# Performance work log

Hardware: AMD Instinct MI355X
Metric: run time of the kernel (lower is better)

Reference implementation:

```python
import jax, jax.numpy as jnp
import numpy as np

N_NODES = 100000


def setup_inputs() -> dict:
    key = jax.random.key(0)
    k1, k2, k3 = jax.random.split(key, 3)
    embedding = jax.random.normal(k1, (N_NODES, 128), dtype=jnp.float32)
    # xavier-ish scale for 128-dim fan-in
    weights = jax.random.normal(k2, (2, 4, 128, 128), dtype=jnp.float32) * 0.088
    biases = jnp.zeros((2, 4, 128), dtype=jnp.float32)
    edges = jax.random.randint(k3, (4, 2, 150000), 0, N_NODES, dtype=jnp.int32)
    return {"embedding": embedding, "weights": weights, "biases": biases, "edges": edges}


def _hetero_conv(h, W, b, edges, n_nodes):
    """HeteroGraphConv(mean) over R relations; each GraphConv uses norm='both'.
    h: [N, d_in], W: [R, d_in, d_h], b: [R, d_h], edges: [R, 2, E]."""

    def per_rel(e, Wr, br):
        src, dst = e[0], e[1]
        ones = jnp.ones(src.shape, dtype=h.dtype)
        deg_out = jnp.maximum(jax.ops.segment_sum(ones, src, num_segments=n_nodes), 1.0)
        deg_in = jnp.maximum(jax.ops.segment_sum(ones, dst, num_segments=n_nodes), 1.0)
        # D_src^{-1/2} X W
        x = h * jax.lax.rsqrt(deg_out)[:, None]
        m = x @ Wr  # [N, d_h]
        # gather along edges, scatter-add to dst (A @ m)
        agg = jax.ops.segment_sum(m[src], dst, num_segments=n_nodes)
        return agg * jax.lax.rsqrt(deg_in)[:, None] + br

    outs = jax.vmap(per_rel)(edges, W, b)  # [R, N, d_h]
    return outs.mean(axis=0)


def reference(embedding, weights, biases, edges):
    n_nodes = embedding.shape[0]
    num_layers = weights.shape[0]
    h = embedding
    for i in range(num_layers):
        out = _hetero_conv(h, weights[i], biases[i], edges, n_nodes)
        out = jax.nn.leaky_relu(out, negative_slope=0.2)
        if i > 0:
            out = out + h  # residual (hidden == in, slice [:, :hidden] is identity)
        h = out
    return h
```

## Files before the change

kernel.cpp:

```cpp
#include <hip/hip_runtime.h>
#include <cstdint>
#include <cstddef>

#define N_NODES 100000
#define D 128
#define R 4
#define NE 150000
#define LAYERS 2
#define NROWS (R * N_NODES)
#define CAP 16
#define TILES (N_NODES / 16)
#define GRID 256
#define TPB 512

typedef __attribute__((ext_vector_type(8))) short bf16x8;
typedef __attribute__((ext_vector_type(4))) float f32x4;
typedef __attribute__((ext_vector_type(4))) int i32x4;
typedef __attribute__((ext_vector_type(4))) unsigned short u16x4;

__device__ __forceinline__ unsigned short f2bf(float x) {
  union { float f; unsigned int u; } v; v.f = x;
  unsigned int u = v.u;
  return (unsigned short)((u + 0x7fffu + ((u >> 16) & 1u)) >> 16);
}
__device__ __forceinline__ float bf2f(unsigned short u) {
  union { unsigned int i; float f; } v; v.i = ((unsigned int)u) << 16;
  return v.f;
}

__global__ void count_kernel(const int* __restrict__ edges, int* __restrict__ deg_i) {
  int e = blockIdx.x * blockDim.x + threadIdx.x;
  int r = blockIdx.y;
  if (e >= NE) return;
  int src = edges[(size_t)(r * 2) * NE + e];
  atomicAdd(&deg_i[r * N_NODES + src], 1);
}

__global__ void fill_kernel(const int* __restrict__ edges, const int* __restrict__ deg_i,
                            int* __restrict__ cursor, int2* __restrict__ rec) {
  int e = blockIdx.x * blockDim.x + threadIdx.x;
  int r = blockIdx.y;
  if (e >= NE) return;
  int src = edges[(size_t)(r * 2) * NE + e];
  int dst = edges[(size_t)(r * 2 + 1) * NE + e];
  float sc = rsqrtf(fmaxf((float)deg_i[r * N_NODES + src], 1.0f));
  int rowg = r * N_NODES + dst;
  int slot = atomicAdd(&cursor[rowg], 1);
  if (slot < CAP) rec[(size_t)rowg * CAP + slot] = make_int2(src, __float_as_int(sc));
}

__global__ void prep_kernel(const float* __restrict__ emb, const float* __restrict__ W,
                            const float* __restrict__ biases, const int* __restrict__ cursor,
                            unsigned short* __restrict__ hb, unsigned short* __restrict__ Wt,
                            float* __restrict__ bmean, float* __restrict__ s_in) {
  int t = blockIdx.x * blockDim.x + threadIdx.x;
  if (t < N_NODES * D / 4) {
    f32x4 v = *(const f32x4*)(emb + (size_t)t * 4);
    u16x4 o;
#pragma unroll
    for (int j = 0; j < 4; ++j) o[j] = f2bf(v[j]);
    *(u16x4*)(hb + (size_t)t * 4) = o;
  }
  if (t < LAYERS * R * D * D) {
    int k = t & 127;
    int c = (t >> 7) & 127;
    int lr = t >> 14;
    Wt[((size_t)lr << 14) | (c << 7) | k] = f2bf(W[((size_t)lr << 14) | (k << 7) | c]);
  }
  if (t < NROWS) s_in[t] = rsqrtf(fmaxf((float)cursor[t], 1.0f));
  if (t < LAYERS * D) {
    int l = t >> 7, cc = t & 127;
    float s = 0.f;
    for (int r = 0; r < R; ++r) s += biases[((size_t)l * R + r) * D + cc];
    bmean[t] = s * 0.25f;
  }
}

__global__ __launch_bounds__(TPB, 2) void fused_kernel(
    const unsigned short* __restrict__ hb,
    const int2* __restrict__ rec,
    const int* __restrict__ cnt,
    const float* __restrict__ s_in,
    const unsigned short* __restrict__ Wt,
    const float* __restrict__ bmean,
    const unsigned short* __restrict__ resid_bf,
    float* __restrict__ out_f,
    unsigned short* __restrict__ out_bf) {
  __shared__ unsigned short t_lds[2][R * 4 * 64 * 8];
  const int w = threadIdx.x >> 6;
  const int lane = threadIdx.x & 63;
  const int m = lane & 15;
  const int q = lane >> 4;
  const int bid = blockIdx.x;
  const int nt = (TILES - bid + GRID - 1) / GRID;

  if (w < 4) {
    const int r = w;
    for (int it = 0; it < nt + 1; ++it) {
      if (it < nt) {
        const int tile = bid + it * GRID;
        const int rowg = r * N_NODES + tile * 16 + m;
        const int2* rp = rec + (size_t)rowg * CAP;
        int n = cnt[rowg];
        n = (n > CAP) ? CAP : n;
        i32x4 r01 = *(const i32x4*)(rp);
        i32x4 r23 = *(const i32x4*)(rp + 2);
        int   srcs[4] = { r01.x, r01.z, r23.x, r23.z };
        float scs[4]  = { __int_as_float(r01.y), __int_as_float(r01.w),
                          __int_as_float(r23.y), __int_as_float(r23.w) };
        float accf[4][8];
#pragma unroll
        for (int ks = 0; ks < 4; ++ks)
#pragma unroll
          for (int j = 0; j < 8; ++j) accf[ks][j] = 0.f;
#pragma unroll
        for (int e = 0; e < 4; ++e) {
          const unsigned short* hp = hb + (size_t)srcs[e] * D + q * 8;
#pragma unroll
          for (int ks = 0; ks < 4; ++ks) {
            bf16x8 a = *(const bf16x8*)(hp + ks * 32);
#pragma unroll
            for (int j = 0; j < 8; ++j)
              accf[ks][j] += scs[e] * bf2f((unsigned short)a[j]);
          }
        }
        for (int i = 4; i < n; i += 2) {
          i32x4 rr = *(const i32x4*)(rp + i);
          float c0 = __int_as_float(rr.y), c1 = __int_as_float(rr.w);
          const unsigned short* h0 = hb + (size_t)rr.x * D + q * 8;
          const unsigned short* h1 = hb + (size_t)rr.z * D + q * 8;
#pragma unroll
          for (int ks = 0; ks < 4; ++ks) {
            bf16x8 a0 = *(const bf16x8*)(h0 + ks * 32);
            bf16x8 a1 = *(const bf16x8*)(h1 + ks * 32);
#pragma unroll
            for (int j = 0; j < 8; ++j)
              accf[ks][j] += c0 * bf2f((unsigned short)a0[j]) + c1 * bf2f((unsigned short)a1[j]);
          }
        }
        unsigned short* dstp = &t_lds[it & 1][(((r * 4) << 6) + lane) * 8];
#pragma unroll
        for (int ks = 0; ks < 4; ++ks) {
          union { bf16x8 v; unsigned short s[8]; } u;
#pragma unroll
          for (int j = 0; j < 8; ++j) u.s[j] = f2bf(accf[ks][j]);
          *(bf16x8*)(dstp + (ks << 6) * 8) = u.v;
        }
      }
      __syncthreads();
    }
  } else {
    const int cw = w - 4;
    bf16x8 breg[R][4][2];
#pragma unroll
    for (int r = 0; r < R; ++r) {
      const unsigned short* wr = Wt + ((size_t)r << 14);
#pragma unroll
      for (int ks = 0; ks < 4; ++ks)
#pragma unroll
        for (int c = 0; c < 2; ++c) {
          int ct = cw * 2 + c;
          breg[r][ks][c] = *(const bf16x8*)(wr + ((ct * 16 + m) << 7) + ks * 32 + q * 8);
        }
    }
    for (int it = 0; it < nt + 1; ++it) {
      if (it > 0) {
        const int tile = bid + (it - 1) * GRID;
        const int pb = (it - 1) & 1;
        float oacc[2][4];
#pragma unroll
        for (int c = 0; c < 2; ++c)
#pragma unroll
          for (int i = 0; i < 4; ++i) oacc[c][i] = 0.f;
#pragma unroll
        for (int r = 0; r < R; ++r) {
          f32x4 acc2[2];
#pragma unroll
          for (int c = 0; c < 2; ++c) acc2[c] = (f32x4){0.f, 0.f, 0.f, 0.f};
#pragma unroll
          for (int ks = 0; ks < 4; ++ks) {
            bf16x8 a = *(const bf16x8*)&t_lds[pb][(((r * 4 + ks) << 6) + lane) * 8];
#pragma unroll
            for (int c = 0; c < 2; ++c)
              acc2[c] = __builtin_amdgcn_mfma_f32_16x16x32_bf16(a, breg[r][ks][c], acc2[c], 0, 0, 0);
          }
          f32x4 s = *(const f32x4*)(s_in + (size_t)r * N_NODES + tile * 16 + q * 4);
#pragma unroll
          for (int c = 0; c < 2; ++c)
#pragma unroll
            for (int i = 0; i < 4; ++i) oacc[c][i] += s[i] * acc2[c][i];
        }
#pragma unroll
        for (int c = 0; c < 2; ++c) {
          int colx = (cw * 2 + c) * 16 + m;
          float bm = bmean[colx];
#pragma unroll
          for (int i = 0; i < 4; ++i) {
            int row = tile * 16 + q * 4 + i;
            float v = oacc[c][i] * 0.25f + bm;
            v = (v >= 0.f) ? v : 0.2f * v;
            if (resid_bf) v += bf2f(resid_bf[(size_t)row * D + colx]);
            if (out_f) out_f[(size_t)row * D + colx] = v;
            else       out_bf[(size_t)row * D + colx] = f2bf(v);
          }
        }
      }
      __syncthreads();
    }
  }
}

extern "C" void kernel_launch(void* const* d_in, const int* in_sizes, int n_in,
                              void* d_out, int out_size, void* d_ws, size_t ws_size,
                              hipStream_t stream) {
  const float* emb    = (const float*)d_in[0];
  const float* W      = (const float*)d_in[1];
  const float* biases = (const float*)d_in[2];
  const int*   edges  = (const int*)d_in[3];
  float* out = (float*)d_out;
  char* ws = (char*)d_ws;

  size_t off = 0;
  auto alloc = [&](size_t bytes) { size_t o = off; off += (bytes + 255) & ~255ull; return o; };
  int* ints      = (int*)(ws + alloc((size_t)2 * NROWS * 4));
  int* deg_i     = ints;
  int* cursor    = ints + NROWS;
  int2* rec      = (int2*)(ws + alloc((size_t)NROWS * CAP * 8));
  size_t zero_bytes = off;
  float* s_in    = (float*)(ws + alloc((size_t)NROWS * 4));
  unsigned short* hb  = (unsigned short*)(ws + alloc((size_t)N_NODES * D * 2));
  unsigned short* hb2 = (unsigned short*)(ws + alloc((size_t)N_NODES * D * 2));
  unsigned short* Wt  = (unsigned short*)(ws + alloc((size_t)LAYERS * R * D * D * 2));
  float* bmean   = (float*)(ws + alloc((size_t)LAYERS * D * 4));
  (void)ws_size;

  hipMemsetAsync(ws, 0, zero_bytes, stream);
  count_kernel<<<dim3((NE + 255) / 256, R), 256, 0, stream>>>(edges, deg_i);
  fill_kernel<<<dim3((NE + 255) / 256, R), 256, 0, stream>>>(edges, deg_i, cursor, rec);
  prep_kernel<<<(N_NODES * D / 4 + 255) / 256, 256, 0, stream>>>(
      emb, W, biases, cursor, hb, Wt, bmean, s_in);

  fused_kernel<<<GRID, TPB, 0, stream>>>(
      hb, rec, cursor, s_in, Wt, bmean, nullptr, nullptr, hb2);
  fused_kernel<<<GRID, TPB, 0, stream>>>(
      hb2, rec, cursor, s_in, Wt + (size_t)R * D * D, bmean + D, hb2, out, nullptr);
}
```

Before: 338.0 us.

## Software-pipeline edge gathers, split CSR into compact head and overflow, merge prep kernels

The gather warps now issue the next tile's neighbour-row loads into registers (double-buffered A/B state) before accumulating the current tile, which hides gather latency. Edge records are split into a compact tile-major 4-slot head array plus an overflow array, so the zeroed workspace is smaller and the common-case record reads are contiguous. Degree counting is folded into the embedding/weight prep kernel, and the s_in precompute is replaced by computing rsqrt from counts inline, which removes a kernel launch and a pass. Barriers become raw s_barrier with explicit lgkmcnt waits. The cost is much higher register pressure in the gather warps.

```diff
diff --git a/kernel.cpp b/kernel.cpp
--- a/kernel.cpp
+++ b/kernel.cpp
@@ -9,6 +9,7 @@
 #define LAYERS 2
 #define NROWS (R * N_NODES)
 #define CAP 16
+#define OVFS 12
 #define TILES (N_NODES / 16)
 #define GRID 256
 #define TPB 512
@@ -28,16 +29,41 @@
   return v.f;
 }
 
-__global__ void count_kernel(const int* __restrict__ edges, int* __restrict__ deg_i) {
-  int e = blockIdx.x * blockDim.x + threadIdx.x;
-  int r = blockIdx.y;
-  if (e >= NE) return;
-  int src = edges[(size_t)(r * 2) * NE + e];
-  atomicAdd(&deg_i[r * N_NODES + src], 1);
+__global__ void prep1_kernel(const float* __restrict__ emb, const float* __restrict__ W,
+                             const float* __restrict__ biases, const int* __restrict__ edges,
+                             int* __restrict__ deg_i, unsigned short* __restrict__ hb,
+                             unsigned short* __restrict__ Wt, float* __restrict__ bmean) {
+  int t = blockIdx.x * blockDim.x + threadIdx.x;
+  if (t < N_NODES * D / 4) {
+    f32x4 v = *(const f32x4*)(emb + (size_t)t * 4);
+    u16x4 o;
+#pragma unroll
+    for (int j = 0; j < 4; ++j) o[j] = f2bf(v[j]);
+    *(u16x4*)(hb + (size_t)t * 4) = o;
+  }
+  if (t < NE * R) {
+    int r = t / NE;
+    int e = t - r * NE;
+    int src = edges[(size_t)(r * 2) * NE + e];
+    atomicAdd(&deg_i[r * N_NODES + src], 1);
+  }
+  if (t < LAYERS * R * D * D) {
+    int k = t & 127;
+    int c = (t >> 7) & 127;
+    int lr = t >> 14;
+    Wt[((size_t)lr << 14) | (c << 7) | k] = f2bf(W[((size_t)lr << 14) | (k << 7) | c]);
+  }
+  if (t < LAYERS * D) {
+    int l = t >> 7, cc = t & 127;
+    float s = 0.f;
+    for (int r = 0; r < R; ++r) s += biases[((size_t)l * R + r) * D + cc];
+    bmean[t] = s * 0.25f;
+  }
 }
 
 __global__ void fill_kernel(const int* __restrict__ edges, const int* __restrict__ deg_i,
-                            int* __restrict__ cursor, int2* __restrict__ rec) {
+                            int* __restrict__ cursor, int2* __restrict__ rec2,
+                            int2* __restrict__ ovf) {
   int e = blockIdx.x * blockDim.x + threadIdx.x;
   int r = blockIdx.y;
   if (e >= NE) return;
@@ -46,41 +72,114 @@
   float sc = rsqrtf(fmaxf((float)deg_i[r * N_NODES + src], 1.0f));
   int rowg = r * N_NODES + dst;
   int slot = atomicAdd(&cursor[rowg], 1);
-  if (slot < CAP) rec[(size_t)rowg * CAP + slot] = make_int2(src, __float_as_int(sc));
-}
-
-__global__ void prep_kernel(const float* __restrict__ emb, const float* __restrict__ W,
-                            const float* __restrict__ biases, const int* __restrict__ cursor,
-                            unsigned short* __restrict__ hb, unsigned short* __restrict__ Wt,
-                            float* __restrict__ bmean, float* __restrict__ s_in) {
-  int t = blockIdx.x * blockDim.x + threadIdx.x;
-  if (t < N_NODES * D / 4) {
-    f32x4 v = *(const f32x4*)(emb + (size_t)t * 4);
-    u16x4 o;
-#pragma unroll
-    for (int j = 0; j < 4; ++j) o[j] = f2bf(v[j]);
-    *(u16x4*)(hb + (size_t)t * 4) = o;
-  }
-  if (t < LAYERS * R * D * D) {
-    int k = t & 127;
-    int c = (t >> 7) & 127;
-    int lr = t >> 14;
-    Wt[((size_t)lr << 14) | (c << 7) | k] = f2bf(W[((size_t)lr << 14) | (k << 7) | c]);
-  }
-  if (t < NROWS) s_in[t] = rsqrtf(fmaxf((float)cursor[t], 1.0f));
-  if (t < LAYERS * D) {
-    int l = t >> 7, cc = t & 127;
-    float s = 0.f;
-    for (int r = 0; r < R; ++r) s += biases[((size_t)l * R + r) * D + cc];
-    bmean[t] = s * 0.25f;
-  }
-}
+  if (slot < 4) {
+    int tile = dst >> 4, mm = dst & 15;
+    rec2[(((size_t)(r * TILES + tile) * 16 + mm) << 2) + slot] = make_int2(src, __float_as_int(sc));
+  } else if (slot < CAP) {
+    ovf[(size_t)rowg * OVFS + (slot - 4)] = make_int2(src, __float_as_int(sc));
+  }
+}
+
+#define DECL_ST(P) \
+  bf16x8 P##g0, P##g1, P##g2, P##g3, P##g4, P##g5, P##g6, P##g7, \
+         P##g8, P##g9, P##g10, P##g11, P##g12, P##g13, P##g14, P##g15; \
+  float P##c0 = 0.f, P##c1 = 0.f, P##c2 = 0.f, P##c3 = 0.f; \
+  i32x4 P##tr = (i32x4){0, 0, 0, 0}; \
+  int P##n = 0
+
+#define P_LOADREC(CN, R0V, R1V, TT) do { \
+  const int2* rp_ = rec2 + (((size_t)(r * TILES + (TT)) * 16 + m) << 2); \
+  CN = cnt[r * N_NODES + (TT) * 16 + m]; \
+  R0V = *(const i32x4*)(rp_); \
+  R1V = *(const i32x4*)(rp_ + 2); \
+} while (0)
+
+#define P_ISSUE(P, CN, R0V, R1V, TT) do { \
+  int n_ = (CN) > CAP ? CAP : (CN); \
+  int a0_ = (R0V).x, a1_ = (R0V).z, a2_ = (R1V).x, a3_ = (R1V).z; \
+  float b0_ = __int_as_float((R0V).y), b1_ = __int_as_float((R0V).w); \
+  float b2_ = __int_as_float((R1V).y), b3_ = __int_as_float((R1V).w); \
+  if (n_ < 1) { a0_ = 0; b0_ = 0.f; } \
+  if (n_ < 2) { a1_ = 0; b1_ = 0.f; } \
+  if (n_ < 3) { a2_ = 0; b2_ = 0.f; } \
+  if (n_ < 4) { a3_ = 0; b3_ = 0.f; } \
+  const unsigned short* h0_ = hb + (size_t)a0_ * D + q * 8; \
+  const unsigned short* h1_ = hb + (size_t)a1_ * D + q * 8; \
+  const unsigned short* h2_ = hb + (size_t)a2_ * D + q * 8; \
+  const unsigned short* h3_ = hb + (size_t)a3_ * D + q * 8; \
+  P##g0  = *(const bf16x8*)(h0_);      P##g1  = *(const bf16x8*)(h0_ + 32); \
+  P##g2  = *(const bf16x8*)(h0_ + 64); P##g3  = *(const bf16x8*)(h0_ + 96); \
+  P##g4  = *(const bf16x8*)(h1_);      P##g5  = *(const bf16x8*)(h1_ + 32); \
+  P##g6  = *(const bf16x8*)(h1_ + 64); P##g7  = *(const bf16x8*)(h1_ + 96); \
+  P##g8  = *(const bf16x8*)(h2_);      P##g9  = *(const bf16x8*)(h2_ + 32); \
+  P##g10 = *(const bf16x8*)(h2_ + 64); P##g11 = *(const bf16x8*)(h2_ + 96); \
+  P##g12 = *(const bf16x8*)(h3_);      P##g13 = *(const bf16x8*)(h3_ + 32); \
+  P##g14 = *(const bf16x8*)(h3_ + 64); P##g15 = *(const bf16x8*)(h3_ + 96); \
+  P##c0 = b0_; P##c1 = b1_; P##c2 = b2_; P##c3 = b3_; P##n = n_; \
+  if (__builtin_expect(n_ > 4, 0)) \
+    P##tr = *(const i32x4*)(ovf + (size_t)(r * N_NODES + (TT) * 16 + m) * OVFS); \
+} while (0)
+
+#define P_ACCUM(P, TT, DSTP) do { \
+  float accf[4][8]; \
+  _Pragma("unroll") for (int k_ = 0; k_ < 4; ++k_) \
+    _Pragma("unroll") for (int j_ = 0; j_ < 8; ++j_) accf[k_][j_] = 0.f; \
+  if (__builtin_expect(P##n > 4, 0)) { \
+    bool ok_ = P##n > 5; \
+    int sA_ = P##tr.x, sB_ = ok_ ? P##tr.z : 0; \
+    float cA_ = __int_as_float(P##tr.y), cB_ = ok_ ? __int_as_float(P##tr.w) : 0.f; \
+    const unsigned short* hA_ = hb + (size_t)sA_ * D + q * 8; \
+    const unsigned short* hB_ = hb + (size_t)sB_ * D + q * 8; \
+    _Pragma("unroll") for (int k_ = 0; k_ < 4; ++k_) { \
+      bf16x8 x0_ = *(const bf16x8*)(hA_ + k_ * 32); \
+      bf16x8 x1_ = *(const bf16x8*)(hB_ + k_ * 32); \
+      _Pragma("unroll") for (int j_ = 0; j_ < 8; ++j_) \
+        accf[k_][j_] += cA_ * bf2f((unsigned short)x0_[j_]) + cB_ * bf2f((unsigned short)x1_[j_]); \
+    } \
+    const int2* op_ = ovf + (size_t)(r * N_NODES + (TT) * 16 + m) * OVFS; \
+    for (int i_ = 6; i_ < P##n; i_ += 2) { \
+      i32x4 rr_ = *(const i32x4*)(op_ + (i_ - 4)); \
+      bool o2_ = (i_ + 1) < P##n; \
+      int s0_ = rr_.x, s1_ = o2_ ? rr_.z : 0; \
+      float d0_ = __int_as_float(rr_.y), d1_ = o2_ ? __int_as_float(rr_.w) : 0.f; \
+      const unsigned short* y0_ = hb + (size_t)s0_ * D + q * 8; \
+      const unsigned short* y1_ = hb + (size_t)s1_ * D + q * 8; \
+      _Pragma("unroll") for (int k_ = 0; k_ < 4; ++k_) { \
+        bf16x8 x0_ = *(const bf16x8*)(y0_ + k_ * 32); \
+        bf16x8 x1_ = *(const bf16x8*)(y1_ + k_ * 32); \
+        _Pragma("unroll") for (int j_ = 0; j_ < 8; ++j_) \
+          accf[k_][j_] += d0_ * bf2f((unsigned short)x0_[j_]) + d1_ * bf2f((unsigned short)x1_[j_]); \
+      } \
+    } \
+  } \
+  _Pragma("unroll") for (int j_ = 0; j_ < 8; ++j_) { \
+    accf[0][j_] += P##c0 * bf2f((unsigned short)P##g0[j_])  + P##c1 * bf2f((unsigned short)P##g4[j_]) \
+                 + P##c2 * bf2f((unsigned short)P##g8[j_])  + P##c3 * bf2f((unsigned short)P##g12[j_]); \
+    accf[1][j_] += P##c0 * bf2f((unsigned short)P##g1[j_])  + P##c1 * bf2f((unsigned short)P##g5[j_]) \
+                 + P##c2 * bf2f((unsigned short)P##g9[j_])  + P##c3 * bf2f((unsigned short)P##g13[j_]); \
+    accf[2][j_] += P##c0 * bf2f((unsigned short)P##g2[j_])  + P##c1 * bf2f((unsigned short)P##g6[j_]) \
+                 + P##c2 * bf2f((unsigned short)P##g10[j_]) + P##c3 * bf2f((unsigned short)P##g14[j_]); \
+    accf[3][j_] += P##c0 * bf2f((unsigned short)P##g3[j_])  + P##c1 * bf2f((unsigned short)P##g7[j_]) \
+                 + P##c2 * bf2f((unsigned short)P##g11[j_]) + P##c3 * bf2f((unsigned short)P##g15[j_]); \
+  } \
+  _Pragma("unroll") for (int k_ = 0; k_ < 4; ++k_) { \
+    union { bf16x8 v; unsigned short s[8]; } u_; \
+    _Pragma("unroll") for (int j_ = 0; j_ < 8; ++j_) u_.s[j_] = f2bf(accf[k_][j_]); \
+    *(bf16x8*)((DSTP) + (k_ << 6) * 8) = u_.v; \
+  } \
+} while (0)
+
+#define P_BARRIER() do { \
+  asm volatile("s_waitcnt lgkmcnt(0)"); \
+  __builtin_amdgcn_sched_barrier(0); \
+  __builtin_amdgcn_s_barrier(); \
+} while (0)
 
 __global__ __launch_bounds__(TPB, 2) void fused_kernel(
     const unsigned short* __restrict__ hb,
-    const int2* __restrict__ rec,
+    const int2* __restrict__ rec2,
+    const int2* __restrict__ ovf,
     const int* __restrict__ cnt,
-    const float* __restrict__ s_in,
     const unsigned short* __restrict__ Wt,
     const float* __restrict__ bmean,
     const unsigned short* __restrict__ resid_bf,
@@ -96,59 +195,42 @@
 
   if (w < 4) {
     const int r = w;
-    for (int it = 0; it < nt + 1; ++it) {
-      if (it < nt) {
-        const int tile = bid + it * GRID;
-        const int rowg = r * N_NODES + tile * 16 + m;
-        const int2* rp = rec + (size_t)rowg * CAP;
-        int n = cnt[rowg];
-        n = (n > CAP) ? CAP : n;
-        i32x4 r01 = *(const i32x4*)(rp);
-        i32x4 r23 = *(const i32x4*)(rp + 2);
-        int   srcs[4] = { r01.x, r01.z, r23.x, r23.z };
-        float scs[4]  = { __int_as_float(r01.y), __int_as_float(r01.w),
-                          __int_as_float(r23.y), __int_as_float(r23.w) };
-        float accf[4][8];
-#pragma unroll
-        for (int ks = 0; ks < 4; ++ks)
-#pragma unroll
-          for (int j = 0; j < 8; ++j) accf[ks][j] = 0.f;
-#pragma unroll
-        for (int e = 0; e < 4; ++e) {
-          const unsigned short* hp = hb + (size_t)srcs[e] * D + q * 8;
-#pragma unroll
-          for (int ks = 0; ks < 4; ++ks) {
-            bf16x8 a = *(const bf16x8*)(hp + ks * 32);
-#pragma unroll
-            for (int j = 0; j < 8; ++j)
-              accf[ks][j] += scs[e] * bf2f((unsigned short)a[j]);
-          }
-        }
-        for (int i = 4; i < n; i += 2) {
-          i32x4 rr = *(const i32x4*)(rp + i);
-          float c0 = __int_as_float(rr.y), c1 = __int_as_float(rr.w);
-          const unsigned short* h0 = hb + (size_t)rr.x * D + q * 8;
-          const unsigned short* h1 = hb + (size_t)rr.z * D + q * 8;
-#pragma unroll
-          for (int ks = 0; ks < 4; ++ks) {
-            bf16x8 a0 = *(const bf16x8*)(h0 + ks * 32);
-            bf16x8 a1 = *(const bf16x8*)(h1 + ks * 32);
-#pragma unroll
-            for (int j = 0; j < 8; ++j)
-              accf[ks][j] += c0 * bf2f((unsigned short)a0[j]) + c1 * bf2f((unsigned short)a1[j]);
-          }
+    DECL_ST(A);
+    DECL_ST(B);
+    int cnA = 0, cnB = 0;
+    i32x4 ra0, ra1, rb0, rb1;
+
+    P_LOADREC(cnA, ra0, ra1, bid);
+    P_ISSUE(A, cnA, ra0, ra1, bid);
+    if (nt > 1) P_LOADREC(cnB, rb0, rb1, bid + GRID);
+
+    int it = 0;
+    for (;;) {
+      {
+        const int tcur = bid + it * GRID;
+        if (it + 1 < nt) {
+          P_ISSUE(B, cnB, rb0, rb1, tcur + GRID);
+          if (it + 2 < nt) P_LOADREC(cnA, ra0, ra1, tcur + 2 * GRID);
         }
         unsigned short* dstp = &t_lds[it & 1][(((r * 4) << 6) + lane) * 8];
-#pragma unroll
-        for (int ks = 0; ks < 4; ++ks) {
-          union { bf16x8 v; unsigned short s[8]; } u;
-#pragma unroll
-          for (int j = 0; j < 8; ++j) u.s[j] = f2bf(accf[ks][j]);
-          *(bf16x8*)(dstp + (ks << 6) * 8) = u.v;
-        }
+        P_ACCUM(A, tcur, dstp);
+        P_BARRIER();
+        if (++it >= nt) break;
       }
-      __syncthreads();
+      {
+        const int tcur = bid + it * GRID;
+        if (it + 1 < nt) {
+          P_ISSUE(A, cnA, ra0, ra1, tcur + GRID);
+          if (it + 2 < nt) P_LOADREC(cnB, rb0, rb1, tcur + 2 * GRID);
+        }
+        unsigned short* dstp = &t_lds[it & 1][(((r * 4) << 6) + lane) * 8];
+        P_ACCUM(B, tcur, dstp);
+        P_BARRIER();
+        if (++it >= nt) break;
+      }
     }
+    asm volatile("s_waitcnt lgkmcnt(0)");
+    __builtin_amdgcn_s_barrier();
   } else {
     const int cw = w - 4;
     bf16x8 breg[R][4][2];
@@ -184,11 +266,12 @@
             for (int c = 0; c < 2; ++c)
               acc2[c] = __builtin_amdgcn_mfma_f32_16x16x32_bf16(a, breg[r][ks][c], acc2[c], 0, 0, 0);
           }
-          f32x4 s = *(const f32x4*)(s_in + (size_t)r * N_NODES + tile * 16 + q * 4);
+          i32x4 ci = *(const i32x4*)(cnt + (size_t)r * N_NODES + tile * 16 + q * 4);
 #pragma unroll
           for (int c = 0; c < 2; ++c)
 #pragma unroll
-            for (int i = 0; i < 4; ++i) oacc[c][i] += s[i] * acc2[c][i];
+            for (int i = 0; i < 4; ++i)
+              oacc[c][i] += rsqrtf(fmaxf((float)ci[i], 1.0f)) * acc2[c][i];
         }
 #pragma unroll
         for (int c = 0; c < 2; ++c) {
@@ -205,7 +288,8 @@
           }
         }
       }
-      __syncthreads();
+      asm volatile("s_waitcnt lgkmcnt(0)");
+      __builtin_amdgcn_s_barrier();
     }
   }
 }
@@ -225,9 +309,9 @@
   int* ints      = (int*)(ws + alloc((size_t)2 * NROWS * 4));
   int* deg_i     = ints;
   int* cursor    = ints + NROWS;
-  int2* rec      = (int2*)(ws + alloc((size_t)NROWS * CAP * 8));
   size_t zero_bytes = off;
-  float* s_in    = (float*)(ws + alloc((size_t)NROWS * 4));
+  int2* rec2     = (int2*)(ws + alloc((size_t)R * TILES * 16 * 4 * 8));
+  int2* ovf      = (int2*)(ws + alloc((size_t)NROWS * OVFS * 8));
   unsigned short* hb  = (unsigned short*)(ws + alloc((size_t)N_NODES * D * 2));
   unsigned short* hb2 = (unsigned short*)(ws + alloc((size_t)N_NODES * D * 2));
   unsigned short* Wt  = (unsigned short*)(ws + alloc((size_t)LAYERS * R * D * D * 2));
@@ -235,13 +319,12 @@
   (void)ws_size;
 
   hipMemsetAsync(ws, 0, zero_bytes, stream);
-  count_kernel<<<dim3((NE + 255) / 256, R), 256, 0, stream>>>(edges, deg_i);
-  fill_kernel<<<dim3((NE + 255) / 256, R), 256, 0, stream>>>(edges, deg_i, cursor, rec);
-  prep_kernel<<<(N_NODES * D / 4 + 255) / 256, 256, 0, stream>>>(
-      emb, W, biases, cursor, hb, Wt, bmean, s_in);
+  prep1_kernel<<<(N_NODES * D / 4 + 255) / 256, 256, 0, stream>>>(
+      emb, W, biases, edges, deg_i, hb, Wt, bmean);
+  fill_kernel<<<dim3((NE + 255) / 256, R), 256, 0, stream>>>(edges, deg_i, cursor, rec2, ovf);
 
   fused_kernel<<<GRID, TPB, 0, stream>>>(
-      hb, rec, cursor, s_in, Wt, bmean, nullptr, nullptr, hb2);
+      hb, rec2, ovf, cursor, Wt, bmean, nullptr, nullptr, hb2);
   fused_kernel<<<GRID, TPB, 0, stream>>>(
-      hb2, rec, cursor, s_in, Wt + (size_t)R * D * D, bmean + D, hb2, out, nullptr);
-}
+      hb2, rec2, ovf, cursor, Wt + (size_t)R * D * D, bmean + D, hb2, out, nullptr);
+}
```

After: 363.8 us. +7.6%, slower.

## Merge all stages into one cooperative kernel with grid syncs and compact edge records

Applied to the files above, without the earlier changes.

Replaces the memset, count, fill, prep and two layer kernels with a single cooperative mega-kernel that uses grid-wide syncs between phases. Edge records are split into a compact 4-slot per-row array plus an overflow buffer, which removes the 16-slot padded reads. The first four gathers are issued up front with masking to improve memory-level parallelism. The in-degree normalisation is computed on the fly from counts instead of a precomputed array. In exchange, the setup phases now run on only 256 blocks, and each grid sync adds a cost.

```diff
diff --git a/kernel.cpp b/kernel.cpp
--- a/kernel.cpp
+++ b/kernel.cpp
@@ -1,6 +1,9 @@
 #include <hip/hip_runtime.h>
+#include <hip/hip_cooperative_groups.h>
 #include <cstdint>
 #include <cstddef>
+
+namespace cg = cooperative_groups;
 
 #define N_NODES 100000
 #define D 128
@@ -9,9 +12,11 @@
 #define LAYERS 2
 #define NROWS (R * N_NODES)
 #define CAP 16
+#define OVFS 12
 #define TILES (N_NODES / 16)
 #define GRID 256
 #define TPB 512
+#define NTH (GRID * TPB)
 
 typedef __attribute__((ext_vector_type(8))) short bf16x8;
 typedef __attribute__((ext_vector_type(4))) float f32x4;
@@ -28,64 +33,64 @@
   return v.f;
 }
 
-__global__ void count_kernel(const int* __restrict__ edges, int* __restrict__ deg_i) {
-  int e = blockIdx.x * blockDim.x + threadIdx.x;
-  int r = blockIdx.y;
-  if (e >= NE) return;
-  int src = edges[(size_t)(r * 2) * NE + e];
-  atomicAdd(&deg_i[r * N_NODES + src], 1);
-}
-
-__global__ void fill_kernel(const int* __restrict__ edges, const int* __restrict__ deg_i,
-                            int* __restrict__ cursor, int2* __restrict__ rec) {
-  int e = blockIdx.x * blockDim.x + threadIdx.x;
-  int r = blockIdx.y;
-  if (e >= NE) return;
-  int src = edges[(size_t)(r * 2) * NE + e];
-  int dst = edges[(size_t)(r * 2 + 1) * NE + e];
-  float sc = rsqrtf(fmaxf((float)deg_i[r * N_NODES + src], 1.0f));
-  int rowg = r * N_NODES + dst;
-  int slot = atomicAdd(&cursor[rowg], 1);
-  if (slot < CAP) rec[(size_t)rowg * CAP + slot] = make_int2(src, __float_as_int(sc));
-}
-
-__global__ void prep_kernel(const float* __restrict__ emb, const float* __restrict__ W,
-                            const float* __restrict__ biases, const int* __restrict__ cursor,
-                            unsigned short* __restrict__ hb, unsigned short* __restrict__ Wt,
-                            float* __restrict__ bmean, float* __restrict__ s_in) {
-  int t = blockIdx.x * blockDim.x + threadIdx.x;
-  if (t < N_NODES * D / 4) {
-    f32x4 v = *(const f32x4*)(emb + (size_t)t * 4);
+__global__ __launch_bounds__(TPB, 2) void mega_kernel(
+    const float* __restrict__ emb, const float* __restrict__ W,
+    const float* __restrict__ biases, const int* __restrict__ edges,
+    int* __restrict__ ints,
+    int2* __restrict__ rec2,
+    int2* __restrict__ ovf,
+    unsigned short* __restrict__ hb,
+    unsigned short* __restrict__ hb2,
+    unsigned short* __restrict__ Wt,
+    float* __restrict__ bmean,
+    float* __restrict__ out) {
+  cg::grid_group grid = cg::this_grid();
+  int* deg_i = ints;
+  int* cursor = ints + NROWS;
+  const int tid = blockIdx.x * TPB + threadIdx.x;
+
+  for (int i = tid; i < 2 * NROWS; i += NTH) ints[i] = 0;
+  grid.sync();
+
+  for (int i = tid; i < NE * R; i += NTH) {
+    int r = i / NE, e = i - r * NE;
+    atomicAdd(&deg_i[r * N_NODES + edges[(size_t)(r * 2) * NE + e]], 1);
+  }
+  for (int i = tid; i < N_NODES * D / 4; i += NTH) {
+    f32x4 v = *(const f32x4*)(emb + (size_t)i * 4);
     u16x4 o;
 #pragma unroll
     for (int j = 0; j < 4; ++j) o[j] = f2bf(v[j]);
-    *(u16x4*)(hb + (size_t)t * 4) = o;
-  }
-  if (t < LAYERS * R * D * D) {
-    int k = t & 127;
-    int c = (t >> 7) & 127;
-    int lr = t >> 14;
+    *(u16x4*)(hb + (size_t)i * 4) = o;
+  }
+  for (int i = tid; i < LAYERS * R * D * D; i += NTH) {
+    int k = i & 127, c = (i >> 7) & 127, lr = i >> 14;
     Wt[((size_t)lr << 14) | (c << 7) | k] = f2bf(W[((size_t)lr << 14) | (k << 7) | c]);
   }
-  if (t < NROWS) s_in[t] = rsqrtf(fmaxf((float)cursor[t], 1.0f));
-  if (t < LAYERS * D) {
-    int l = t >> 7, cc = t & 127;
+  if (tid < LAYERS * D) {
+    int l = tid >> 7, cc = tid & 127;
     float s = 0.f;
     for (int r = 0; r < R; ++r) s += biases[((size_t)l * R + r) * D + cc];
-    bmean[t] = s * 0.25f;
-  }
-}
-
-__global__ __launch_bounds__(TPB, 2) void fused_kernel(
-    const unsigned short* __restrict__ hb,
-    const int2* __restrict__ rec,
-    const int* __restrict__ cnt,
-    const float* __restrict__ s_in,
-    const unsigned short* __restrict__ Wt,
-    const float* __restrict__ bmean,
-    const unsigned short* __restrict__ resid_bf,
-    float* __restrict__ out_f,
-    unsigned short* __restrict__ out_bf) {
+    bmean[tid] = s * 0.25f;
+  }
+  grid.sync();
+
+  for (int i = tid; i < NE * R; i += NTH) {
+    int r = i / NE, e = i - r * NE;
+    int src = edges[(size_t)(r * 2) * NE + e];
+    int dst = edges[(size_t)(r * 2 + 1) * NE + e];
+    float sc = rsqrtf(fmaxf((float)deg_i[r * N_NODES + src], 1.0f));
+    int rowg = r * N_NODES + dst;
+    int slot = atomicAdd(&cursor[rowg], 1);
+    if (slot < 4) {
+      rec2[(((size_t)(r * TILES + (dst >> 4)) * 16 + (dst & 15)) << 2) + slot] =
+          make_int2(src, __float_as_int(sc));
+    } else if (slot < CAP) {
+      ovf[(size_t)rowg * OVFS + (slot - 4)] = make_int2(src, __float_as_int(sc));
+    }
+  }
+  grid.sync();
+
   __shared__ unsigned short t_lds[2][R * 4 * 64 * 8];
   const int w = threadIdx.x >> 6;
   const int lane = threadIdx.x & 63;
@@ -93,120 +98,165 @@
   const int q = lane >> 4;
   const int bid = blockIdx.x;
   const int nt = (TILES - bid + GRID - 1) / GRID;
-
-  if (w < 4) {
-    const int r = w;
-    for (int it = 0; it < nt + 1; ++it) {
-      if (it < nt) {
-        const int tile = bid + it * GRID;
-        const int rowg = r * N_NODES + tile * 16 + m;
-        const int2* rp = rec + (size_t)rowg * CAP;
-        int n = cnt[rowg];
-        n = (n > CAP) ? CAP : n;
-        i32x4 r01 = *(const i32x4*)(rp);
-        i32x4 r23 = *(const i32x4*)(rp + 2);
-        int   srcs[4] = { r01.x, r01.z, r23.x, r23.z };
-        float scs[4]  = { __int_as_float(r01.y), __int_as_float(r01.w),
-                          __int_as_float(r23.y), __int_as_float(r23.w) };
-        float accf[4][8];
+  const int* cnt = cursor;
+
+  for (int L = 0; L < LAYERS; ++L) {
+    const unsigned short* hin = L ? hb2 : hb;
+
+    if (w < 4) {
+      const int r = w;
+      for (int it = 0; it < nt + 1; ++it) {
+        if (it < nt) {
+          const int tile = bid + it * GRID;
+          const int rowg = r * N_NODES + tile * 16 + m;
+          const int2* rp = rec2 + (((size_t)(r * TILES + tile) * 16 + m) << 2);
+          int cn = cnt[rowg];
+          int n = cn > CAP ? CAP : cn;
+          i32x4 r01 = *(const i32x4*)rp;
+          i32x4 r23 = *(const i32x4*)(rp + 2);
+          int s0 = r01.x, s1 = r01.z, s2 = r23.x, s3 = r23.z;
+          float c0 = __int_as_float(r01.y), c1 = __int_as_float(r01.w);
+          float c2 = __int_as_float(r23.y), c3 = __int_as_float(r23.w);
+          if (n < 1) { s0 = 0; c0 = 0.f; }
+          if (n < 2) { s1 = 0; c1 = 0.f; }
+          if (n < 3) { s2 = 0; c2 = 0.f; }
+          if (n < 4) { s3 = 0; c3 = 0.f; }
+          const unsigned short* h0 = hin + (size_t)s0 * D + q * 8;
+          const unsigned short* h1 = hin + (size_t)s1 * D + q * 8;
+          const unsigned short* h2 = hin + (size_t)s2 * D + q * 8;
+          const unsigned short* h3 = hin + (size_t)s3 * D + q * 8;
+          bf16x8 g0  = *(const bf16x8*)(h0);      bf16x8 g1  = *(const bf16x8*)(h0 + 32);
+          bf16x8 g2  = *(const bf16x8*)(h0 + 64); bf16x8 g3  = *(const bf16x8*)(h0 + 96);
+          bf16x8 g4  = *(const bf16x8*)(h1);      bf16x8 g5  = *(const bf16x8*)(h1 + 32);
+          bf16x8 g6  = *(const bf16x8*)(h1 + 64); bf16x8 g7  = *(const bf16x8*)(h1 + 96);
+          bf16x8 g8  = *(const bf16x8*)(h2);      bf16x8 g9  = *(const bf16x8*)(h2 + 32);
+          bf16x8 g10 = *(const bf16x8*)(h2 + 64); bf16x8 g11 = *(const bf16x8*)(h2 + 96);
+          bf16x8 g12 = *(const bf16x8*)(h3);      bf16x8 g13 = *(const bf16x8*)(h3 + 32);
+          bf16x8 g14 = *(const bf16x8*)(h3 + 64); bf16x8 g15 = *(const bf16x8*)(h3 + 96);
+          float accf[4][8];
+#pragma unroll
+          for (int ks = 0; ks < 4; ++ks)
+#pragma unroll
+            for (int j = 0; j < 8; ++j) accf[ks][j] = 0.f;
+          if (__builtin_expect(n > 4, 0)) {
+            const int2* op = ovf + (size_t)rowg * OVFS;
+            i32x4 tr = *(const i32x4*)op;
+            bool ok = n > 5;
+            int sA = tr.x, sB = ok ? tr.z : 0;
+            float cA = __int_as_float(tr.y), cB = ok ? __int_as_float(tr.w) : 0.f;
+            const unsigned short* hA = hin + (size_t)sA * D + q * 8;
+            const unsigned short* hB = hin + (size_t)sB * D + q * 8;
+#pragma unroll
+            for (int k2 = 0; k2 < 4; ++k2) {
+              bf16x8 x0 = *(const bf16x8*)(hA + k2 * 32);
+              bf16x8 x1 = *(const bf16x8*)(hB + k2 * 32);
+#pragma unroll
+              for (int j = 0; j < 8; ++j)
+                accf[k2][j] += cA * bf2f((unsigned short)x0[j]) + cB * bf2f((unsigned short)x1[j]);
+            }
+            for (int i2 = 6; i2 < n; i2 += 2) {
+              i32x4 rr = *(const i32x4*)(op + (i2 - 4));
+              bool o2 = (i2 + 1) < n;
+              int t0 = rr.x, t1 = o2 ? rr.z : 0;
+              float d0 = __int_as_float(rr.y), d1 = o2 ? __int_as_float(rr.w) : 0.f;
+              const unsigned short* y0 = hin + (size_t)t0 * D + q * 8;
+              const unsigned short* y1 = hin + (size_t)t1 * D + q * 8;
+#pragma unroll
+              for (int k2 = 0; k2 < 4; ++k2) {
+                bf16x8 x0 = *(const bf16x8*)(y0 + k2 * 32);
+                bf16x8 x1 = *(const bf16x8*)(y1 + k2 * 32);
+#pragma unroll
+                for (int j = 0; j < 8; ++j)
+                  accf[k2][j] += d0 * bf2f((unsigned short)x0[j]) + d1 * bf2f((unsigned short)x1[j]);
+              }
+            }
+          }
+#pragma unroll
+          for (int j = 0; j < 8; ++j) {
+            accf[0][j] += c0 * bf2f((unsigned short)g0[j]) + c1 * bf2f((unsigned short)g4[j])
+                        + c2 * bf2f((unsigned short)g8[j]) + c3 * bf2f((unsigned short)g12[j]);
+            accf[1][j] += c0 * bf2f((unsigned short)g1[j]) + c1 * bf2f((unsigned short)g5[j])
+                        + c2 * bf2f((unsigned short)g9[j]) + c3 * bf2f((unsigned short)g13[j]);
+            accf[2][j] += c0 * bf2f((unsigned short)g2[j]) + c1 * bf2f((unsigned short)g6[j])
+                        + c2 * bf2f((unsigned short)g10[j]) + c3 * bf2f((unsigned short)g14[j]);
+            accf[3][j] += c0 * bf2f((unsigned short)g3[j]) + c1 * bf2f((unsigned short)g7[j])
+                        + c2 * bf2f((unsigned short)g11[j]) + c3 * bf2f((unsigned short)g15[j]);
+          }
+          unsigned short* dstp = &t_lds[it & 1][(((r * 4) << 6) + lane) * 8];
+#pragma unroll
+          for (int ks = 0; ks < 4; ++ks) {
+            union { bf16x8 v; unsigned short s[8]; } u;
+#pragma unroll
+            for (int j = 0; j < 8; ++j) u.s[j] = f2bf(accf[ks][j]);
+            *(bf16x8*)(dstp + (ks << 6) * 8) = u.v;
+          }
+        }
+        __syncthreads();
+      }
+    } else {
+      const int cw = w - 4;
+      bf16x8 breg[R][4][2];
+#pragma unroll
+      for (int r2 = 0; r2 < R; ++r2) {
+        const unsigned short* wr = Wt + ((size_t)(L * R + r2) << 14);
 #pragma unroll
         for (int ks = 0; ks < 4; ++ks)
 #pragma unroll
-          for (int j = 0; j < 8; ++j) accf[ks][j] = 0.f;
-#pragma unroll
-        for (int e = 0; e < 4; ++e) {
-          const unsigned short* hp = hb + (size_t)srcs[e] * D + q * 8;
-#pragma unroll
-          for (int ks = 0; ks < 4; ++ks) {
-            bf16x8 a = *(const bf16x8*)(hp + ks * 32);
-#pragma unroll
-            for (int j = 0; j < 8; ++j)
-              accf[ks][j] += scs[e] * bf2f((unsigned short)a[j]);
+          for (int c = 0; c < 2; ++c) {
+            int ct = cw * 2 + c;
+            breg[r2][ks][c] = *(const bf16x8*)(wr + ((ct * 16 + m) << 7) + ks * 32 + q * 8);
+          }
+      }
+      for (int it = 0; it < nt + 1; ++it) {
+        if (it > 0) {
+          const int tile = bid + (it - 1) * GRID;
+          const int pb = (it - 1) & 1;
+          float oacc[2][4];
+#pragma unroll
+          for (int c = 0; c < 2; ++c)
+#pragma unroll
+            for (int i = 0; i < 4; ++i) oacc[c][i] = 0.f;
+#pragma unroll
+          for (int r2 = 0; r2 < R; ++r2) {
+            f32x4 acc2[2];
+#pragma unroll
+            for (int c = 0; c < 2; ++c) acc2[c] = (f32x4){0.f, 0.f, 0.f, 0.f};
+#pragma unroll
+            for (int ks = 0; ks < 4; ++ks) {
+              bf16x8 a = *(const bf16x8*)&t_lds[pb][(((r2 * 4 + ks) << 6) + lane) * 8];
+#pragma unroll
+              for (int c = 0; c < 2; ++c)
+                acc2[c] = __builtin_amdgcn_mfma_f32_16x16x32_bf16(a, breg[r2][ks][c], acc2[c], 0, 0, 0);
+            }
+            i32x4 ci = *(const i32x4*)(cnt + (size_t)r2 * N_NODES + tile * 16 + q * 4);
+#pragma unroll
+            for (int c = 0; c < 2; ++c)
+#pragma unroll
+              for (int i = 0; i < 4; ++i)
+                oacc[c][i] += rsqrtf(fmaxf((float)ci[i], 1.0f)) * acc2[c][i];
+          }
+#pragma unroll
+          for (int c = 0; c < 2; ++c) {
+            int colx = (cw * 2 + c) * 16 + m;
+            float bm = bmean[L * D + colx];
+#pragma unroll
+            for (int i = 0; i < 4; ++i) {
+              int row = tile * 16 + q * 4 + i;
+              float v = oacc[c][i] * 0.25f + bm;
+              v = (v >= 0.f) ? v : 0.2f * v;
+              if (L == 0) {
+                hb2[(size_t)row * D + colx] = f2bf(v);
+              } else {
+                v += bf2f(hb2[(size_t)row * D + colx]);
+                out[(size_t)row * D + colx] = v;
+              }
+            }
           }
         }
-        for (int i = 4; i < n; i += 2) {
-          i32x4 rr = *(const i32x4*)(rp + i);
-          float c0 = __int_as_float(rr.y), c1 = __int_as_float(rr.w);
-          const unsigned short* h0 = hb + (size_t)rr.x * D + q * 8;
-          const unsigned short* h1 = hb + (size_t)rr.z * D + q * 8;
-#pragma unroll
-          for (int ks = 0; ks < 4; ++ks) {
-            bf16x8 a0 = *(const bf16x8*)(h0 + ks * 32);
-            bf16x8 a1 = *(const bf16x8*)(h1 + ks * 32);
-#pragma unroll
-            for (int j = 0; j < 8; ++j)
-              accf[ks][j] += c0 * bf2f((unsigned short)a0[j]) + c1 * bf2f((unsigned short)a1[j]);
-          }
-        }
-        unsigned short* dstp = &t_lds[it & 1][(((r * 4) << 6) + lane) * 8];
-#pragma unroll
-        for (int ks = 0; ks < 4; ++ks) {
-          union { bf16x8 v; unsigned short s[8]; } u;
-#pragma unroll
-          for (int j = 0; j < 8; ++j) u.s[j] = f2bf(accf[ks][j]);
-          *(bf16x8*)(dstp + (ks << 6) * 8) = u.v;
-        }
+        __syncthreads();
       }
-      __syncthreads();
     }
-  } else {
-    const int cw = w - 4;
-    bf16x8 breg[R][4][2];
-#pragma unroll
-    for (int r = 0; r < R; ++r) {
-      const unsigned short* wr = Wt + ((size_t)r << 14);
-#pragma unroll
-      for (int ks = 0; ks < 4; ++ks)
-#pragma unroll
-        for (int c = 0; c < 2; ++c) {
-          int ct = cw * 2 + c;
-          breg[r][ks][c] = *(const bf16x8*)(wr + ((ct * 16 + m) << 7) + ks * 32 + q * 8);
-        }
-    }
-    for (int it = 0; it < nt + 1; ++it) {
-      if (it > 0) {
-        const int tile = bid + (it - 1) * GRID;
-        const int pb = (it - 1) & 1;
-        float oacc[2][4];
-#pragma unroll
-        for (int c = 0; c < 2; ++c)
-#pragma unroll
-          for (int i = 0; i < 4; ++i) oacc[c][i] = 0.f;
-#pragma unroll
-        for (int r = 0; r < R; ++r) {
-          f32x4 acc2[2];
-#pragma unroll
-          for (int c = 0; c < 2; ++c) acc2[c] = (f32x4){0.f, 0.f, 0.f, 0.f};
-#pragma unroll
-          for (int ks = 0; ks < 4; ++ks) {
-            bf16x8 a = *(const bf16x8*)&t_lds[pb][(((r * 4 + ks) << 6) + lane) * 8];
-#pragma unroll
-            for (int c = 0; c < 2; ++c)
-              acc2[c] = __builtin_amdgcn_mfma_f32_16x16x32_bf16(a, breg[r][ks][c], acc2[c], 0, 0, 0);
-          }
-          f32x4 s = *(const f32x4*)(s_in + (size_t)r * N_NODES + tile * 16 + q * 4);
-#pragma unroll
-          for (int c = 0; c < 2; ++c)
-#pragma unroll
-            for (int i = 0; i < 4; ++i) oacc[c][i] += s[i] * acc2[c][i];
-        }
-#pragma unroll
-        for (int c = 0; c < 2; ++c) {
-          int colx = (cw * 2 + c) * 16 + m;
-          float bm = bmean[colx];
-#pragma unroll
-          for (int i = 0; i < 4; ++i) {
-            int row = tile * 16 + q * 4 + i;
-            float v = oacc[c][i] * 0.25f + bm;
-            v = (v >= 0.f) ? v : 0.2f * v;
-            if (resid_bf) v += bf2f(resid_bf[(size_t)row * D + colx]);
-            if (out_f) out_f[(size_t)row * D + colx] = v;
-            else       out_bf[(size_t)row * D + colx] = f2bf(v);
-          }
-        }
-      }
-      __syncthreads();
-    }
+    if (L == 0) grid.sync();
   }
 }
 
@@ -222,26 +272,17 @@
 
   size_t off = 0;
   auto alloc = [&](size_t bytes) { size_t o = off; off += (bytes + 255) & ~255ull; return o; };
-  int* ints      = (int*)(ws + alloc((size_t)2 * NROWS * 4));
-  int* deg_i     = ints;
-  int* cursor    = ints + NROWS;
-  int2* rec      = (int2*)(ws + alloc((size_t)NROWS * CAP * 8));
-  size_t zero_bytes = off;
-  float* s_in    = (float*)(ws + alloc((size_t)NROWS * 4));
+  int* ints = (int*)(ws + alloc((size_t)2 * NROWS * 4));
+  int2* rec2 = (int2*)(ws + alloc((size_t)R * TILES * 16 * 4 * 8));
+  int2* ovf  = (int2*)(ws + alloc((size_t)NROWS * OVFS * 8));
   unsigned short* hb  = (unsigned short*)(ws + alloc((size_t)N_NODES * D * 2));
   unsigned short* hb2 = (unsigned short*)(ws + alloc((size_t)N_NODES * D * 2));
   unsigned short* Wt  = (unsigned short*)(ws + alloc((size_t)LAYERS * R * D * D * 2));
-  float* bmean   = (float*)(ws + alloc((size_t)LAYERS * D * 4));
+  float* bmean = (float*)(ws + alloc((size_t)LAYERS * D * 4));
   (void)ws_size;
 
-  hipMemsetAsync(ws, 0, zero_bytes, stream);
-  count_kernel<<<dim3((NE + 255) / 256, R), 256, 0, stream>>>(edges, deg_i);
-  fill_kernel<<<dim3((NE + 255) / 256, R), 256, 0, stream>>>(edges, deg_i, cursor, rec);
-  prep_kernel<<<(N_NODES * D / 4 + 255) / 256, 256, 0, stream>>>(
-      emb, W, biases, cursor, hb, Wt, bmean, s_in);
-
-  fused_kernel<<<GRID, TPB, 0, stream>>>(
-      hb, rec, cursor, s_in, Wt, bmean, nullptr, nullptr, hb2);
-  fused_kernel<<<GRID, TPB, 0, stream>>>(
-      hb2, rec, cursor, s_in, Wt + (size_t)R * D * D, bmean + D, hb2, out, nullptr);
-}
+  void* kargs[] = { (void*)&emb, (void*)&W, (void*)&biases, (void*)&edges,
+                    (void*)&ints, (void*)&rec2, (void*)&ovf, (void*)&hb, (void*)&hb2,
+                    (void*)&Wt, (void*)&bmean, (void*)&out };
+  hipLaunchCooperativeKernel((void*)mega_kernel, dim3(GRID), dim3(TPB), kargs, 0, stream);
+}
```

New measurement: 470.3 us. +39.1%, slower.
